# Optimization experiments

Measured on AMD Instinct MI355X. Metric: run time of the kernel, lower is better.

## Reference

```python
import jax, jax.numpy as jnp
import numpy as np
from jax import lax

B, S, I = 128, 256, 128          # batch, seq_len, input_size
CTX, OUT = 256, 128              # context_input_size, output_size
CPM, NM = 1024, 4                # center_size_per_module, num_modules
CENTER = NM * CPM
IN_SIZES = [I + CTX, CTX, CTX, CTX]          # only module 0 sees the input
HID = [CPM, CPM, CPM, CPM + OUT]             # last module also emits output


def setup_inputs() -> dict:
    key = jax.random.key(0)
    ks = jax.random.split(key, 4 + 5 * NM)
    d = {
        "inputs": jax.random.normal(ks[0], (B, 1, S, I), jnp.float32),
        "center_init": jax.random.normal(ks[1], (NM, B, CPM), jnp.float32),
        "mod_init": jax.random.normal(ks[2], (NM - 1, B, CPM), jnp.float32),
        "mod_init_last": jax.random.normal(ks[3], (B, CPM + OUT), jnp.float32),
    }
    for i in range(NM):
        k = ks[4 + 5 * i: 4 + 5 * (i + 1)]
        d[f"pm{i}"] = jax.random.normal(k[0], (CENTER, CTX), jnp.float32) * 0.02
        d[f"wih{i}"] = jax.random.normal(k[1], (3 * HID[i], IN_SIZES[i]), jnp.float32) * 0.05
        d[f"whh{i}"] = jax.random.normal(k[2], (3 * HID[i], HID[i]), jnp.float32) * 0.05
        d[f"bih{i}"] = jnp.zeros((3 * HID[i],), jnp.float32)
        d[f"bhh{i}"] = jnp.zeros((3 * HID[i],), jnp.float32)
    return d


def _gru(x, h, wih, whh, bih, bhh):
    # PyTorch GRUCell semantics
    gi = x @ wih.T + bih
    gh = h @ whh.T + bhh
    ir, iz, inn = jnp.split(gi, 3, axis=1)
    hr, hz, hn = jnp.split(gh, 3, axis=1)
    r = jax.nn.sigmoid(ir + hr)
    z = jax.nn.sigmoid(iz + hz)
    n = jnp.tanh(inn + r * hn)
    return (1.0 - z) * n + z * h


def _forward(inputs, center_init, mod_init, mod_init_last, pms, wihs, whhs, bihs, bhhs):
    xs = jnp.swapaxes(inputs[:, 0], 0, 1)  # [S, B, I]

    def step(carry, x_t):
        centers, mods, mod_last = carry  # [NM,B,CPM], [NM-1,B,CPM], [B,CPM+OUT]
        # torch.cat(prev_center_states, dim=1): module-major concat -> [B, NM*CPM]
        center_state = jnp.reshape(jnp.swapaxes(centers, 0, 1), (centers.shape[1], -1))
        new_centers, new_mods = [], []
        out = new_mod_last = None
        for i in range(NM):
            ctx = center_state @ pms[i]                       # [B, CTX]
            xin = jnp.concatenate([x_t, ctx], axis=1) if i == 0 else ctx
            h_prev = mod_last if i == NM - 1 else mods[i]
            h = _gru(xin, h_prev, wihs[i], whhs[i], bihs[i], bhhs[i])
            if i == NM - 1:
                out = h[:, :OUT]                              # split([output, center_feat])
                new_centers.append(h[:, OUT:])
                new_mod_last = h
            else:
                new_centers.append(h)
                new_mods.append(h)
        return (jnp.stack(new_centers), jnp.stack(new_mods), new_mod_last), out

    _, ys = lax.scan(step, (center_init, mod_init, mod_init_last), xs)
    return jnp.swapaxes(ys, 0, 1)  # [B, S, OUT]


def reference(inputs, center_init, mod_init, mod_init_last,
              pm0, pm1, pm2, pm3,
              wih0, wih1, wih2, wih3,
              whh0, whh1, whh2, whh3,
              bih0, bih1, bih2, bih3,
              bhh0, bhh1, bhh2, bhh3):
    return _forward(inputs, center_init, mod_init, mod_init_last,
                    (pm0, pm1, pm2, pm3),
                    (wih0, wih1, wih2, wih3),
                    (whh0, whh1, whh2, whh3),
                    (bih0, bih1, bih2, bih3),
                    (bhh0, bhh1, bhh2, bhh3))
```

## Files before the change

### kernel.cpp

```cpp
#include <hip/hip_runtime.h>
#include <hip/hip_bf16.h>

typedef _Float16 f16;
typedef f16  f16x8 __attribute__((ext_vector_type(8)));
typedef float f32x4 __attribute__((ext_vector_type(4)));

__device__ __forceinline__ f16x8 ld8h(const f16* p){ return *reinterpret_cast<const f16x8*>(p); }
__device__ __forceinline__ void fsplit(float x, f16* hi, f16* lo){
    f16 h=(f16)x; *hi=h; *lo=(f16)((x-(float)h)*4096.0f);
}
__device__ __forceinline__ size_t fragoff(int n, int k, int Kc){
    return ((size_t)(n>>4)*Kc + (k>>5))*512 + (size_t)((((k&31)>>3)*16 + (n&15))*8 + (k&7));
}

constexpr size_t NXE   = 128ull*256*128;
constexpr size_t NPM   = 1024ull*4096;
constexpr size_t NWIH0 = 3072ull*384;
constexpr size_t NWIH12= 3072ull*256;
constexpr size_t NWIH3 = 3456ull*256;
constexpr size_t NWHH  = 3072ull*1024;
constexpr size_t NWHH3 = 3456ull*1152;
constexpr size_t NCEN  = 128ull*4096;
constexpr size_t NCTX  = 128ull*1024;
constexpr size_t NHMX  = 128ull*1152;

constexpr size_t OFF_XH    = 0;
constexpr size_t OFF_XL    = OFF_XH + NXE*2;
constexpr size_t OFF_PMH   = OFF_XL + NXE*2;
constexpr size_t OFF_PML   = OFF_PMH + NPM*2;
constexpr size_t OFF_WIHH0 = OFF_PML + NPM*2;
constexpr size_t OFF_WIHH1 = OFF_WIHH0 + NWIH0*2;
constexpr size_t OFF_WIHH2 = OFF_WIHH1 + NWIH12*2;
constexpr size_t OFF_WIHH3 = OFF_WIHH2 + NWIH12*2;
constexpr size_t OFF_WIHL0 = OFF_WIHH3 + NWIH3*2;
constexpr size_t OFF_WIHL1 = OFF_WIHL0 + NWIH0*2;
constexpr size_t OFF_WIHL2 = OFF_WIHL1 + NWIH12*2;
constexpr size_t OFF_WIHL3 = OFF_WIHL2 + NWIH12*2;
constexpr size_t OFF_WHHH0 = OFF_WIHL3 + NWIH3*2;
constexpr size_t OFF_WHHH1 = OFF_WHHH0 + NWHH*2;
constexpr size_t OFF_WHHH2 = OFF_WHHH1 + NWHH*2;
constexpr size_t OFF_WHHH3 = OFF_WHHH2 + NWHH*2;
constexpr size_t OFF_WHHL0 = OFF_WHHH3 + NWHH3*2;
constexpr size_t OFF_WHHL1 = OFF_WHHL0 + NWHH*2;
constexpr size_t OFF_WHHL2 = OFF_WHHL1 + NWHH*2;
constexpr size_t OFF_WHHL3 = OFF_WHHL2 + NWHH*2;
constexpr size_t OFF_CENH  = OFF_WHHL3 + NWHH3*2;
constexpr size_t OFF_CENL  = OFF_CENH + 2*NCEN*2;
constexpr size_t OFF_CTXH  = OFF_CENL + 2*NCEN*2;
constexpr size_t OFF_CTXL  = OFF_CTXH + NCTX*2;
constexpr size_t OFF_HH    = OFF_CTXL + NCTX*2;
constexpr size_t OFF_HL    = OFF_HH + 8*NHMX*2;
constexpr size_t OFF_HF    = OFF_HL + 8*NHMX*2;
constexpr size_t WS_NEED   = OFF_HF + 8*NHMX*4;

__device__ __forceinline__ f16* hh_ptr(char* ws,int p,int i){ return (f16*)(ws+OFF_HH+((size_t)(p*4+i))*NHMX*2); }
__device__ __forceinline__ f16* hl_ptr(char* ws,int p,int i){ return (f16*)(ws+OFF_HL+((size_t)(p*4+i))*NHMX*2); }
__device__ __forceinline__ float* hf_ptr(char* ws,int p,int i){ return (float*)(ws+OFF_HF+((size_t)(p*4+i))*NHMX*4); }

__global__ void k_repack_w(const float* __restrict__ src, f16* __restrict__ hi,
                           f16* __restrict__ lo, int K){
    int n = blockIdx.x;
    const float* row = src + (size_t)n*K;
    int Kc = K >> 5;
    for (int k8 = threadIdx.x*8; k8 < K; k8 += 2048) {
        f16x8 hv, lv;
        #pragma unroll
        for (int e = 0; e < 8; ++e) { f16 a,b; fsplit(row[k8+e], &a, &b); hv[e]=a; lv[e]=b; }
        size_t d = fragoff(n, k8, Kc);
        *reinterpret_cast<f16x8*>(hi + d) = hv;
        *reinterpret_cast<f16x8*>(lo + d) = lv;
    }
}

__global__ void k_repack_pm(const float* __restrict__ p0, const float* __restrict__ p1,
                            const float* __restrict__ p2, const float* __restrict__ p3,
                            f16* __restrict__ hi, f16* __restrict__ lo){
    int k0 = blockIdx.x * 8;
    for (int c = threadIdx.x; c < 1024; c += 256) {
        int i = c >> 8, nl = c & 255;
        const float* p = (i==0?p0 : i==1?p1 : i==2?p2 : p3);
        f16x8 hv, lv;
        #pragma unroll
        for (int e = 0; e < 8; ++e) { f16 a,b; fsplit(p[(size_t)(k0+e)*256 + nl], &a, &b); hv[e]=a; lv[e]=b; }
        #pragma unroll
        for (int e = 0; e < 8; ++e) { size_t d = fragoff(c, k0+e, 128); hi[d]=hv[e]; lo[d]=lv[e]; }
    }
}

__global__ void k_repack_x(const float* __restrict__ src, f16* __restrict__ hi, f16* __restrict__ lo){
    size_t g = ((size_t)blockIdx.x*256 + threadIdx.x) * 8;
    if (g >= NXE) return;
    int m = (int)(g >> 15), t = (int)((g >> 7) & 255), d0 = (int)(g & 127);
    f16x8 hv, lv;
    #pragma unroll
    for (int e = 0; e < 8; ++e) { f16 a,b; fsplit(src[g+e], &a, &b); hv[e]=a; lv[e]=b; }
    size_t d = (size_t)t*16384 + fragoff(m, d0, 4);
    *reinterpret_cast<f16x8*>(hi + d) = hv;
    *reinterpret_cast<f16x8*>(lo + d) = lv;
}

__global__ void k_init_cen(const float* __restrict__ ci, char* ws){
    size_t g = ((size_t)blockIdx.x*256 + threadIdx.x) * 8;
    if (g >= 4ull*128*1024) return;
    int i = (int)(g >> 17), b = (int)((g >> 10) & 127), c = (int)(g & 1023);
    f16* hi = (f16*)(ws + OFF_CENH);
    f16* lo = (f16*)(ws + OFF_CENL);
    f16x8 hv, lv;
    #pragma unroll
    for (int e = 0; e < 8; ++e) { f16 a,bb; fsplit(ci[g+e], &a, &bb); hv[e]=a; lv[e]=bb; }
    size_t d = fragoff(b, i*1024 + c, 128);
    *reinterpret_cast<f16x8*>(hi + d) = hv;
    *reinterpret_cast<f16x8*>(lo + d) = lv;
}

__global__ void k_init_mod(const float* __restrict__ mi, char* ws){
    size_t g = ((size_t)blockIdx.x*256 + threadIdx.x) * 8;
    if (g >= 3ull*128*1024) return;
    int i = (int)(g >> 17), b = (int)((g >> 10) & 127), j = (int)(g & 1023);
    float* hf = hf_ptr(ws, 0, i);
    f16 *hh = hh_ptr(ws, 0, i), *hl = hl_ptr(ws, 0, i);
    f16x8 hv, lv;
    #pragma unroll
    for (int e = 0; e < 8; ++e) {
        float v = mi[g+e]; hf[(size_t)b*1024 + j + e] = v;
        f16 a,bb; fsplit(v, &a, &bb); hv[e]=a; lv[e]=bb;
    }
    size_t d = fragoff(b, j, 32);
    *reinterpret_cast<f16x8*>(hh + d) = hv;
    *reinterpret_cast<f16x8*>(hl + d) = lv;
}

__global__ void k_init_last(const float* __restrict__ ml, char* ws){
    int b = blockIdx.x;
    float* hf = hf_ptr(ws, 0, 3);
    f16 *hh = hh_ptr(ws, 0, 3), *hl = hl_ptr(ws, 0, 3);
    for (int j = threadIdx.x*8; j < 1152; j += 2048) {
        f16x8 hv, lv;
        #pragma unroll
        for (int e = 0; e < 8; ++e) {
            float v = ml[(size_t)b*1152 + j + e]; hf[(size_t)b*1152 + j + e] = v;
            f16 a,bb; fsplit(v, &a, &bb); hv[e]=a; lv[e]=bb;
        }
        size_t d = fragoff(b, j, 36);
        *reinterpret_cast<f16x8*>(hh + d) = hv;
        *reinterpret_cast<f16x8*>(hl + d) = lv;
    }
}

__global__ __launch_bounds__(512) void k_ctx(char* ws, int par){
    __shared__ float red[8][32][17];
    const f16* cenh = (const f16*)(ws + OFF_CENH) + (size_t)par*NCEN;
    const f16* cenl = (const f16*)(ws + OFF_CENL) + (size_t)par*NCEN;
    const f16* pmh  = (const f16*)(ws + OFF_PMH);
    const f16* pml  = (const f16*)(ws + OFF_PML);
    int tid = threadIdx.x, lane = tid & 63, wv = tid >> 6;
    int bm = blockIdx.x >> 6, bn = blockIdx.x & 63;
    size_t lb = (size_t)lane*8;
    size_t a0 = ((size_t)(bm*2)*128 + wv*16)*512 + lb;
    size_t a1 = a0 + 128*512;
    size_t bb = ((size_t)bn*128 + wv*16)*512 + lb;
    f32x4 h0={},h1={},c0={},c1={};
    #pragma unroll 4
    for (int kc = 0; kc < 16; ++kc) {
        f16x8 bh = ld8h(pmh + bb + kc*512), bl = ld8h(pml + bb + kc*512);
        f16x8 ah0 = ld8h(cenh + a0 + kc*512), al0 = ld8h(cenl + a0 + kc*512);
        f16x8 ah1 = ld8h(cenh + a1 + kc*512), al1 = ld8h(cenl + a1 + kc*512);
        h0 = __builtin_amdgcn_mfma_f32_16x16x32_f16(ah0, bh, h0, 0,0,0);
        c0 = __builtin_amdgcn_mfma_f32_16x16x32_f16(al0, bh, c0, 0,0,0);
        c0 = __builtin_amdgcn_mfma_f32_16x16x32_f16(ah0, bl, c0, 0,0,0);
        h1 = __builtin_amdgcn_mfma_f32_16x16x32_f16(ah1, bh, h1, 0,0,0);
        c1 = __builtin_amdgcn_mfma_f32_16x16x32_f16(al1, bh, c1, 0,0,0);
        c1 = __builtin_amdgcn_mfma_f32_16x16x32_f16(ah1, bl, c1, 0,0,0);
    }
    int rg = lane >> 4, fr = lane & 15;
    const float inv = 1.0f/4096.0f;
    #pragma unroll
    for (int rr = 0; rr < 4; ++rr) {
        red[wv][rg*4+rr][fr]      = h0[rr] + c0[rr]*inv;
        red[wv][16+rg*4+rr][fr]   = h1[rr] + c1[rr]*inv;
    }
    __syncthreads();
    int r = tid >> 4, c = tid & 15;
    float s = red[0][r][c]+red[1][r][c]+red[2][r][c]+red[3][r][c]
            + red[4][r][c]+red[5][r][c]+red[6][r][c]+red[7][r][c];
    int m = bm*32 + r, n = bn*16 + c;
    size_t d = fragoff(m, n, 32);
    f16* ctxh = (f16*)(ws + OFF_CTXH);
    f16* ctxl = (f16*)(ws + OFF_CTXL);
    fsplit(s, &ctxh[d], &ctxl[d]);
}

__global__ __launch_bounds__(256) void k_fused(char* ws,
    const float* __restrict__ bih0, const float* __restrict__ bih1,
    const float* __restrict__ bih2, const float* __restrict__ bih3,
    const float* __restrict__ bhh0, const float* __restrict__ bhh1,
    const float* __restrict__ bhh2, const float* __restrict__ bhh3,
    float* __restrict__ out, int t, int par)
{
    int tid = threadIdx.x, lane = tid & 63, wv = tid >> 6;
    int fr = lane & 15, rg = lane >> 4;
    int tile = blockIdx.x;
    int i, jt;
    if (tile < 64)       { i = 0; jt = tile; }
    else if (tile < 128) { i = 1; jt = tile - 64; }
    else if (tile < 192) { i = 2; jt = tile - 128; }
    else                 { i = 3; jt = tile - 192; }
    const int H  = (i == 3) ? 1152 : 1024;
    const int K1 = (i == 0) ? 384 : 256;
    const int Kc1 = K1 >> 5, KcH = H >> 5, Ht = H >> 4;

    const f16* WihH = (const f16*)(ws + (i==0?OFF_WIHH0 : i==1?OFF_WIHH1 : i==2?OFF_WIHH2 : OFF_WIHH3));
    const f16* WihL = (const f16*)(ws + (i==0?OFF_WIHL0 : i==1?OFF_WIHL1 : i==2?OFF_WIHL2 : OFF_WIHL3));
    const f16* WhhH = (const f16*)(ws + (i==0?OFF_WHHH0 : i==1?OFF_WHHH1 : i==2?OFF_WHHH2 : OFF_WHHH3));
    const f16* WhhL = (const f16*)(ws + (i==0?OFF_WHHL0 : i==1?OFF_WHHL1 : i==2?OFF_WHHL2 : OFF_WHHL3));

    size_t lb = (size_t)lane*8;
    size_t b1[3], b2[3];
    #pragma unroll
    for (int s = 0; s < 3; ++s) {
        b1[s] = ((size_t)(s*Ht + jt)*Kc1)*512 + lb;
        b2[s] = ((size_t)(s*Ht + jt)*KcH)*512 + lb;
    }
    int mt0 = wv*2;
    f32x4 aRh[2]={{},{}}, aRc[2]={{},{}}, aZh[2]={{},{}}, aZc[2]={{},{}};
    f32x4 aIh[2]={{},{}}, aIc[2]={{},{}}, aNh[2]={{},{}}, aNc[2]={{},{}};

    {
        const f16* XH_ = (const f16*)(ws + OFF_XH);
        const f16* XL_ = (const f16*)(ws + OFF_XL);
        const f16* CH_ = (const f16*)(ws + OFF_CTXH);
        const f16* CL_ = (const f16*)(ws + OFF_CTXL);
        size_t xb0 = ((size_t)(t*8 + mt0)*4)*512 + lb, xb1 = xb0 + 4*512;
        size_t cb0 = ((size_t)mt0*32)*512 + lb,        cb1 = cb0 + 32*512;
        #pragma unroll 2
        for (int kc = 0; kc < Kc1; ++kc) {
            f16x8 ah0, al0, ah1, al1;
            if (i == 0 && kc < 4) {
                ah0 = ld8h(XH_ + xb0 + kc*512); al0 = ld8h(XL_ + xb0 + kc*512);
                ah1 = ld8h(XH_ + xb1 + kc*512); al1 = ld8h(XL_ + xb1 + kc*512);
            } else {
                int ck = (i == 0) ? kc - 4 : i*8 + kc;
                ah0 = ld8h(CH_ + cb0 + ck*512); al0 = ld8h(CL_ + cb0 + ck*512);
                ah1 = ld8h(CH_ + cb1 + ck*512); al1 = ld8h(CL_ + cb1 + ck*512);
            }
            f16x8 bh, bl;
            bh = ld8h(WihH + b1[0] + kc*512); bl = ld8h(WihL + b1[0] + kc*512);
            aRh[0] = __builtin_amdgcn_mfma_f32_16x16x32_f16(ah0, bh, aRh[0],0,0,0);
            aRc[0] = __builtin_amdgcn_mfma_f32_16x16x32_f16(al0, bh, aRc[0],0,0,0);
            aRc[0] = __builtin_amdgcn_mfma_f32_16x16x32_f16(ah0, bl, aRc[0],0,0,0);
            aRh[1] = __builtin_amdgcn_mfma_f32_16x16x32_f16(ah1, bh, aRh[1],0,0,0);
            aRc[1] = __builtin_amdgcn_mfma_f32_16x16x32_f16(al1, bh, aRc[1],0,0,0);
            aRc[1] = __builtin_amdgcn_mfma_f32_16x16x32_f16(ah1, bl, aRc[1],0,0,0);
            bh = ld8h(WihH + b1[1] + kc*512); bl = ld8h(WihL + b1[1] + kc*512);
            aZh[0] = __builtin_amdgcn_mfma_f32_16x16x32_f16(ah0, bh, aZh[0],0,0,0);
            aZc[0] = __builtin_amdgcn_mfma_f32_16x16x32_f16(al0, bh, aZc[0],0,0,0);
            aZc[0] = __builtin_amdgcn_mfma_f32_16x16x32_f16(ah0, bl, aZc[0],0,0,0);
            aZh[1] = __builtin_amdgcn_mfma_f32_16x16x32_f16(ah1, bh, aZh[1],0,0,0);
            aZc[1] = __builtin_amdgcn_mfma_f32_16x16x32_f16(al1, bh, aZc[1],0,0,0);
            aZc[1] = __builtin_amdgcn_mfma_f32_16x16x32_f16(ah1, bl, aZc[1],0,0,0);
            bh = ld8h(WihH + b1[2] + kc*512); bl = ld8h(WihL + b1[2] + kc*512);
            aIh[0] = __builtin_amdgcn_mfma_f32_16x16x32_f16(ah0, bh, aIh[0],0,0,0);
            aIc[0] = __builtin_amdgcn_mfma_f32_16x16x32_f16(al0, bh, aIc[0],0,0,0);
            aIc[0] = __builtin_amdgcn_mfma_f32_16x16x32_f16(ah0, bl, aIc[0],0,0,0);
            aIh[1] = __builtin_amdgcn_mfma_f32_16x16x32_f16(ah1, bh, aIh[1],0,0,0);
            aIc[1] = __builtin_amdgcn_mfma_f32_16x16x32_f16(al1, bh, aIc[1],0,0,0);
            aIc[1] = __builtin_amdgcn_mfma_f32_16x16x32_f16(ah1, bl, aIc[1],0,0,0);
        }
    }
    {
        const f16* HHp = hh_ptr(ws, par, i);
        const f16* HLp = hl_ptr(ws, par, i);
        size_t hb0 = ((size_t)mt0*KcH)*512 + lb, hb1 = hb0 + (size_t)KcH*512;
        #pragma unroll 2
        for (int kc = 0; kc < KcH; ++kc) {
            f16x8 ah0 = ld8h(HHp + hb0 + kc*512), al0 = ld8h(HLp + hb0 + kc*512);
            f16x8 ah1 = ld8h(HHp + hb1 + kc*512), al1 = ld8h(HLp + hb1 + kc*512);
            f16x8 bh, bl;
            bh = ld8h(WhhH + b2[0] + kc*512); bl = ld8h(WhhL + b2[0] + kc*512);
            aRh[0] = __builtin_amdgcn_mfma_f32_16x16x32_f16(ah0, bh, aRh[0],0,0,0);
            aRc[0] = __builtin_amdgcn_mfma_f32_16x16x32_f16(al0, bh, aRc[0],0,0,0);
            aRc[0] = __builtin_amdgcn_mfma_f32_16x16x32_f16(ah0, bl, aRc[0],0,0,0);
            aRh[1] = __builtin_amdgcn_mfma_f32_16x16x32_f16(ah1, bh, aRh[1],0,0,0);
            aRc[1] = __builtin_amdgcn_mfma_f32_16x16x32_f16(al1, bh, aRc[1],0,0,0);
            aRc[1] = __builtin_amdgcn_mfma_f32_16x16x32_f16(ah1, bl, aRc[1],0,0,0);
            bh = ld8h(WhhH + b2[1] + kc*512); bl = ld8h(WhhL + b2[1] + kc*512);
            aZh[0] = __builtin_amdgcn_mfma_f32_16x16x32_f16(ah0, bh, aZh[0],0,0,0);
            aZc[0] = __builtin_amdgcn_mfma_f32_16x16x32_f16(al0, bh, aZc[0],0,0,0);
            aZc[0] = __builtin_amdgcn_mfma_f32_16x16x32_f16(ah0, bl, aZc[0],0,0,0);
            aZh[1] = __builtin_amdgcn_mfma_f32_16x16x32_f16(ah1, bh, aZh[1],0,0,0);
            aZc[1] = __builtin_amdgcn_mfma_f32_16x16x32_f16(al1, bh, aZc[1],0,0,0);
            aZc[1] = __builtin_amdgcn_mfma_f32_16x16x32_f16(ah1, bl, aZc[1],0,0,0);
            bh = ld8h(WhhH + b2[2] + kc*512); bl = ld8h(WhhL + b2[2] + kc*512);
            aNh[0] = __builtin_amdgcn_mfma_f32_16x16x32_f16(ah0, bh, aNh[0],0,0,0);
            aNc[0] = __builtin_amdgcn_mfma_f32_16x16x32_f16(al0, bh, aNc[0],0,0,0);
            aNc[0] = __builtin_amdgcn_mfma_f32_16x16x32_f16(ah0, bl, aNc[0],0,0,0);
            aNh[1] = __builtin_amdgcn_mfma_f32_16x16x32_f16(ah1, bh, aNh[1],0,0,0);
            aNc[1] = __builtin_amdgcn_mfma_f32_16x16x32_f16(al1, bh, aNc[1],0,0,0);
            aNc[1] = __builtin_amdgcn_mfma_f32_16x16x32_f16(ah1, bl, aNc[1],0,0,0);
        }
    }

    const float* bihp = (i==0?bih0 : i==1?bih1 : i==2?bih2 : bih3);
    const float* bhhp = (i==0?bhh0 : i==1?bhh1 : i==2?bhh2 : bhh3);
    int j = jt*16 + fr;
    float bir = bihp[j], biz = bihp[H+j], bin = bihp[2*H+j];
    float bhr = bhhp[j], bhz = bhhp[H+j], bhn = bhhp[2*H+j];
    const float* hfP = hf_ptr(ws, par, i);
    float* hfN = hf_ptr(ws, par^1, i);
    f16 *hhN = hh_ptr(ws, par^1, i), *hlN = hl_ptr(ws, par^1, i);
    f16* cenhN = (f16*)(ws + OFF_CENH) + (size_t)(par^1)*NCEN;
    f16* cenlN = (f16*)(ws + OFF_CENL) + (size_t)(par^1)*NCEN;
    const float inv = 1.0f/4096.0f;
    #pragma unroll
    for (int mf = 0; mf < 2; ++mf) {
        #pragma unroll
        for (int rr = 0; rr < 4; ++rr) {
            float r_ = aRh[mf][rr] + aRc[mf][rr]*inv + bir + bhr;
            float z_ = aZh[mf][rr] + aZc[mf][rr]*inv + biz + bhz;
            float in_ = aIh[mf][rr] + aIc[mf][rr]*inv + bin;
            float hn_ = aNh[mf][rr] + aNc[mf][rr]*inv + bhn;
            float rgt = 1.f/(1.f + expf(-r_));
            float zgt = 1.f/(1.f + expf(-z_));
            float ngt = tanhf(in_ + rgt*hn_);
            int m = wv*32 + mf*16 + rg*4 + rr;
            float hp = hfP[(size_t)m*H + j];
            float hnew = (1.f - zgt)*ngt + zgt*hp;
            hfN[(size_t)m*H + j] = hnew;
            size_t hd = fragoff(m, j, KcH);
            fsplit(hnew, &hhN[hd], &hlN[hd]);
            if (i < 3) {
                size_t cd = fragoff(m, i*1024 + j, 128);
                fsplit(hnew, &cenhN[cd], &cenlN[cd]);
            } else if (j >= 128) {
                size_t cd = fragoff(m, 3072 + j - 128, 128);
                fsplit(hnew, &cenhN[cd], &cenlN[cd]);
            } else {
                out[((size_t)m*256 + t)*128 + j] = hnew;
            }
        }
    }
}

extern "C" void kernel_launch(void* const* d_in, const int* in_sizes, int n_in,
                              void* d_out, int out_size, void* d_ws, size_t ws_size,
                              hipStream_t stream)
{
    char* ws = (char*)d_ws;
    const float* inp   = (const float*)d_in[0];
    const float* cini  = (const float*)d_in[1];
    const float* mini  = (const float*)d_in[2];
    const float* mlast = (const float*)d_in[3];
    const float *pm[4], *wih[4], *whh[4], *bih[4], *bhh[4];
    for (int i = 0; i < 4; ++i) {
        pm[i]  = (const float*)d_in[4 + 5*i];
        wih[i] = (const float*)d_in[5 + 5*i];
        whh[i] = (const float*)d_in[6 + 5*i];
        bih[i] = (const float*)d_in[7 + 5*i];
        bhh[i] = (const float*)d_in[8 + 5*i];
    }
    float* out = (float*)d_out;

    k_repack_x<<<2048, 256, 0, stream>>>(inp, (f16*)(ws+OFF_XH), (f16*)(ws+OFF_XL));
    k_repack_pm<<<512, 256, 0, stream>>>(pm[0], pm[1], pm[2], pm[3],
                                         (f16*)(ws+OFF_PMH), (f16*)(ws+OFF_PML));
    k_repack_w<<<3072, 256, 0, stream>>>(wih[0], (f16*)(ws+OFF_WIHH0), (f16*)(ws+OFF_WIHL0), 384);
    k_repack_w<<<3072, 256, 0, stream>>>(wih[1], (f16*)(ws+OFF_WIHH1), (f16*)(ws+OFF_WIHL1), 256);
    k_repack_w<<<3072, 256, 0, stream>>>(wih[2], (f16*)(ws+OFF_WIHH2), (f16*)(ws+OFF_WIHL2), 256);
    k_repack_w<<<3456, 256, 0, stream>>>(wih[3], (f16*)(ws+OFF_WIHH3), (f16*)(ws+OFF_WIHL3), 256);
    k_repack_w<<<3072, 256, 0, stream>>>(whh[0], (f16*)(ws+OFF_WHHH0), (f16*)(ws+OFF_WHHL0), 1024);
    k_repack_w<<<3072, 256, 0, stream>>>(whh[1], (f16*)(ws+OFF_WHHH1), (f16*)(ws+OFF_WHHL1), 1024);
    k_repack_w<<<3072, 256, 0, stream>>>(whh[2], (f16*)(ws+OFF_WHHH2), (f16*)(ws+OFF_WHHL2), 1024);
    k_repack_w<<<3456, 256, 0, stream>>>(whh[3], (f16*)(ws+OFF_WHHH3), (f16*)(ws+OFF_WHHL3), 1152);
    k_init_cen<<<256, 256, 0, stream>>>(cini, ws);
    k_init_mod<<<192, 256, 0, stream>>>(mini, ws);
    k_init_last<<<128, 256, 0, stream>>>(mlast, ws);

    for (int t = 0; t < 256; ++t) {
        int par = t & 1;
        k_ctx<<<256, 512, 0, stream>>>(ws, par);
        k_fused<<<264, 256, 0, stream>>>(ws,
            bih[0], bih[1], bih[2], bih[3],
            bhh[0], bhh[1], bhh[2], bhh[3],
            out, t, par);
    }
    (void)in_sizes; (void)n_in; (void)out_size; (void)ws_size; (void)WS_NEED;
}
```

Baseline: 14.59 ms.

## Replace per-timestep kernel launches with persistent cooperative kernel using grid syncs

Replaces the 512 per-step kernel launches (context matmul plus fused GRU gates) with one cooperative persistent kernel of 512 blocks that loops over all timesteps, separating the phases with grid-wide syncs. Work is re-split so each block computes one 16x16 context tile and half of a gate tile (one 16-row fragment per wave); 16 blocks take an extra gate unit. This is meant to remove launch overhead and the inter-kernel gaps on the serial recurrence. In exchange it adds two grid syncs per step, halves the M-reuse of each loaded weight fragment in the gate phase, and leaves the extra gate units on a few blocks as a tail.

```diff
diff --git a/kernel.cpp b/kernel.cpp
--- a/kernel.cpp
+++ b/kernel.cpp
@@ -1,5 +1,8 @@
 #include <hip/hip_runtime.h>
 #include <hip/hip_bf16.h>
+#include <hip/hip_cooperative_groups.h>
+
+namespace cg = cooperative_groups;
 
 typedef _Float16 f16;
 typedef f16  f16x8 __attribute__((ext_vector_type(8)));
@@ -9,6 +12,7 @@
 __device__ __forceinline__ void fsplit(float x, f16* hi, f16* lo){
     f16 h=(f16)x; *hi=h; *lo=(f16)((x-(float)h)*4096.0f);
 }
+#define MFMA16(a,b,c) __builtin_amdgcn_mfma_f32_16x16x32_f16((a),(b),(c),0,0,0)
 __device__ __forceinline__ size_t fragoff(int n, int k, int Kc){
     return ((size_t)(n>>4)*Kc + (k>>5))*512 + (size_t)((((k&31)>>3)*16 + (n&15))*8 + (k&7));
 }
@@ -79,11 +83,11 @@
     for (int c = threadIdx.x; c < 1024; c += 256) {
         int i = c >> 8, nl = c & 255;
         const float* p = (i==0?p0 : i==1?p1 : i==2?p2 : p3);
-        f16x8 hv, lv;
         #pragma unroll
-        for (int e = 0; e < 8; ++e) { f16 a,b; fsplit(p[(size_t)(k0+e)*256 + nl], &a, &b); hv[e]=a; lv[e]=b; }
-        #pragma unroll
-        for (int e = 0; e < 8; ++e) { size_t d = fragoff(c, k0+e, 128); hi[d]=hv[e]; lo[d]=lv[e]; }
+        for (int e = 0; e < 8; ++e) {
+            f16 a,b; fsplit(p[(size_t)(k0+e)*256 + nl], &a, &b);
+            size_t d = fragoff(c, k0+e, 128); hi[d]=a; lo[d]=b;
+        }
     }
 }
 
@@ -147,59 +151,13 @@
     }
 }
 
-__global__ __launch_bounds__(512) void k_ctx(char* ws, int par){
-    __shared__ float red[8][32][17];
-    const f16* cenh = (const f16*)(ws + OFF_CENH) + (size_t)par*NCEN;
-    const f16* cenl = (const f16*)(ws + OFF_CENL) + (size_t)par*NCEN;
-    const f16* pmh  = (const f16*)(ws + OFF_PMH);
-    const f16* pml  = (const f16*)(ws + OFF_PML);
-    int tid = threadIdx.x, lane = tid & 63, wv = tid >> 6;
-    int bm = blockIdx.x >> 6, bn = blockIdx.x & 63;
-    size_t lb = (size_t)lane*8;
-    size_t a0 = ((size_t)(bm*2)*128 + wv*16)*512 + lb;
-    size_t a1 = a0 + 128*512;
-    size_t bb = ((size_t)bn*128 + wv*16)*512 + lb;
-    f32x4 h0={},h1={},c0={},c1={};
-    #pragma unroll 4
-    for (int kc = 0; kc < 16; ++kc) {
-        f16x8 bh = ld8h(pmh + bb + kc*512), bl = ld8h(pml + bb + kc*512);
-        f16x8 ah0 = ld8h(cenh + a0 + kc*512), al0 = ld8h(cenl + a0 + kc*512);
-        f16x8 ah1 = ld8h(cenh + a1 + kc*512), al1 = ld8h(cenl + a1 + kc*512);
-        h0 = __builtin_amdgcn_mfma_f32_16x16x32_f16(ah0, bh, h0, 0,0,0);
-        c0 = __builtin_amdgcn_mfma_f32_16x16x32_f16(al0, bh, c0, 0,0,0);
-        c0 = __builtin_amdgcn_mfma_f32_16x16x32_f16(ah0, bl, c0, 0,0,0);
-        h1 = __builtin_amdgcn_mfma_f32_16x16x32_f16(ah1, bh, h1, 0,0,0);
-        c1 = __builtin_amdgcn_mfma_f32_16x16x32_f16(al1, bh, c1, 0,0,0);
-        c1 = __builtin_amdgcn_mfma_f32_16x16x32_f16(ah1, bl, c1, 0,0,0);
-    }
-    int rg = lane >> 4, fr = lane & 15;
-    const float inv = 1.0f/4096.0f;
-    #pragma unroll
-    for (int rr = 0; rr < 4; ++rr) {
-        red[wv][rg*4+rr][fr]      = h0[rr] + c0[rr]*inv;
-        red[wv][16+rg*4+rr][fr]   = h1[rr] + c1[rr]*inv;
-    }
-    __syncthreads();
-    int r = tid >> 4, c = tid & 15;
-    float s = red[0][r][c]+red[1][r][c]+red[2][r][c]+red[3][r][c]
-            + red[4][r][c]+red[5][r][c]+red[6][r][c]+red[7][r][c];
-    int m = bm*32 + r, n = bn*16 + c;
-    size_t d = fragoff(m, n, 32);
-    f16* ctxh = (f16*)(ws + OFF_CTXH);
-    f16* ctxl = (f16*)(ws + OFF_CTXL);
-    fsplit(s, &ctxh[d], &ctxl[d]);
-}
-
-__global__ __launch_bounds__(256) void k_fused(char* ws,
-    const float* __restrict__ bih0, const float* __restrict__ bih1,
-    const float* __restrict__ bih2, const float* __restrict__ bih3,
-    const float* __restrict__ bhh0, const float* __restrict__ bhh1,
-    const float* __restrict__ bhh2, const float* __restrict__ bhh3,
-    float* __restrict__ out, int t, int par)
+__device__ __forceinline__ void gates_unit(char* ws,
+    const float* bih0, const float* bih1, const float* bih2, const float* bih3,
+    const float* bhh0, const float* bhh1, const float* bhh2, const float* bhh3,
+    float* out, int t, int par, int u, int lane, int wv)
 {
-    int tid = threadIdx.x, lane = tid & 63, wv = tid >> 6;
-    int fr = lane & 15, rg = lane >> 4;
-    int tile = blockIdx.x;
+    int tile = (u < 512) ? (u >> 1) : (256 + ((u - 512) >> 1));
+    int half = u & 1;
     int i, jt;
     if (tile < 64)       { i = 0; jt = tile; }
     else if (tile < 128) { i = 1; jt = tile - 64; }
@@ -221,85 +179,49 @@
         b1[s] = ((size_t)(s*Ht + jt)*Kc1)*512 + lb;
         b2[s] = ((size_t)(s*Ht + jt)*KcH)*512 + lb;
     }
-    int mt0 = wv*2;
-    f32x4 aRh[2]={{},{}}, aRc[2]={{},{}}, aZh[2]={{},{}}, aZc[2]={{},{}};
-    f32x4 aIh[2]={{},{}}, aIc[2]={{},{}}, aNh[2]={{},{}}, aNc[2]={{},{}};
+    int mf = half*4 + wv;
+
+    f32x4 rh={},rc={},zh={},zc={},inh={},inc={},nhh={},nhc={};
 
     {
         const f16* XH_ = (const f16*)(ws + OFF_XH);
         const f16* XL_ = (const f16*)(ws + OFF_XL);
         const f16* CH_ = (const f16*)(ws + OFF_CTXH);
         const f16* CL_ = (const f16*)(ws + OFF_CTXL);
-        size_t xb0 = ((size_t)(t*8 + mt0)*4)*512 + lb, xb1 = xb0 + 4*512;
-        size_t cb0 = ((size_t)mt0*32)*512 + lb,        cb1 = cb0 + 32*512;
+        size_t xb = ((size_t)(t*8 + mf)*4)*512 + lb;
+        size_t cb = ((size_t)mf*32)*512 + lb;
         #pragma unroll 2
         for (int kc = 0; kc < Kc1; ++kc) {
-            f16x8 ah0, al0, ah1, al1;
-            if (i == 0 && kc < 4) {
-                ah0 = ld8h(XH_ + xb0 + kc*512); al0 = ld8h(XL_ + xb0 + kc*512);
-                ah1 = ld8h(XH_ + xb1 + kc*512); al1 = ld8h(XL_ + xb1 + kc*512);
-            } else {
-                int ck = (i == 0) ? kc - 4 : i*8 + kc;
-                ah0 = ld8h(CH_ + cb0 + ck*512); al0 = ld8h(CL_ + cb0 + ck*512);
-                ah1 = ld8h(CH_ + cb1 + ck*512); al1 = ld8h(CL_ + cb1 + ck*512);
-            }
+            f16x8 ah, al;
+            if (i == 0 && kc < 4) { ah = ld8h(XH_ + xb + kc*512); al = ld8h(XL_ + xb + kc*512); }
+            else { int ck = (i == 0) ? kc - 4 : i*8 + kc;
+                   ah = ld8h(CH_ + cb + ck*512); al = ld8h(CL_ + cb + ck*512); }
             f16x8 bh, bl;
             bh = ld8h(WihH + b1[0] + kc*512); bl = ld8h(WihL + b1[0] + kc*512);
-            aRh[0] = __builtin_amdgcn_mfma_f32_16x16x32_f16(ah0, bh, aRh[0],0,0,0);
-            aRc[0] = __builtin_amdgcn_mfma_f32_16x16x32_f16(al0, bh, aRc[0],0,0,0);
-            aRc[0] = __builtin_amdgcn_mfma_f32_16x16x32_f16(ah0, bl, aRc[0],0,0,0);
-            aRh[1] = __builtin_amdgcn_mfma_f32_16x16x32_f16(ah1, bh, aRh[1],0,0,0);
-            aRc[1] = __builtin_amdgcn_mfma_f32_16x16x32_f16(al1, bh, aRc[1],0,0,0);
-            aRc[1] = __builtin_amdgcn_mfma_f32_16x16x32_f16(ah1, bl, aRc[1],0,0,0);
+            rh = MFMA16(ah,bh,rh); rc = MFMA16(al,bh,rc); rc = MFMA16(ah,bl,rc);
             bh = ld8h(WihH + b1[1] + kc*512); bl = ld8h(WihL + b1[1] + kc*512);
-            aZh[0] = __builtin_amdgcn_mfma_f32_16x16x32_f16(ah0, bh, aZh[0],0,0,0);
-            aZc[0] = __builtin_amdgcn_mfma_f32_16x16x32_f16(al0, bh, aZc[0],0,0,0);
-            aZc[0] = __builtin_amdgcn_mfma_f32_16x16x32_f16(ah0, bl, aZc[0],0,0,0);
-            aZh[1] = __builtin_amdgcn_mfma_f32_16x16x32_f16(ah1, bh, aZh[1],0,0,0);
-            aZc[1] = __builtin_amdgcn_mfma_f32_16x16x32_f16(al1, bh, aZc[1],0,0,0);
-            aZc[1] = __builtin_amdgcn_mfma_f32_16x16x32_f16(ah1, bl, aZc[1],0,0,0);
+            zh = MFMA16(ah,bh,zh); zc = MFMA16(al,bh,zc); zc = MFMA16(ah,bl,zc);
             bh = ld8h(WihH + b1[2] + kc*512); bl = ld8h(WihL + b1[2] + kc*512);
-            aIh[0] = __builtin_amdgcn_mfma_f32_16x16x32_f16(ah0, bh, aIh[0],0,0,0);
-            aIc[0] = __builtin_amdgcn_mfma_f32_16x16x32_f16(al0, bh, aIc[0],0,0,0);
-            aIc[0] = __builtin_amdgcn_mfma_f32_16x16x32_f16(ah0, bl, aIc[0],0,0,0);
-            aIh[1] = __builtin_amdgcn_mfma_f32_16x16x32_f16(ah1, bh, aIh[1],0,0,0);
-            aIc[1] = __builtin_amdgcn_mfma_f32_16x16x32_f16(al1, bh, aIc[1],0,0,0);
-            aIc[1] = __builtin_amdgcn_mfma_f32_16x16x32_f16(ah1, bl, aIc[1],0,0,0);
+            inh = MFMA16(ah,bh,inh); inc = MFMA16(al,bh,inc); inc = MFMA16(ah,bl,inc);
         }
     }
     {
         const f16* HHp = hh_ptr(ws, par, i);
         const f16* HLp = hl_ptr(ws, par, i);
-        size_t hb0 = ((size_t)mt0*KcH)*512 + lb, hb1 = hb0 + (size_t)KcH*512;
+        size_t hb = ((size_t)mf*KcH)*512 + lb;
         #pragma unroll 2
         for (int kc = 0; kc < KcH; ++kc) {
-            f16x8 ah0 = ld8h(HHp + hb0 + kc*512), al0 = ld8h(HLp + hb0 + kc*512);
-            f16x8 ah1 = ld8h(HHp + hb1 + kc*512), al1 = ld8h(HLp + hb1 + kc*512);
+            f16x8 ah = ld8h(HHp + hb + kc*512), al = ld8h(HLp + hb + kc*512);
             f16x8 bh, bl;
             bh = ld8h(WhhH + b2[0] + kc*512); bl = ld8h(WhhL + b2[0] + kc*512);
-            aRh[0] = __builtin_amdgcn_mfma_f32_16x16x32_f16(ah0, bh, aRh[0],0,0,0);
-            aRc[0] = __builtin_amdgcn_mfma_f32_16x16x32_f16(al0, bh, aRc[0],0,0,0);
-            aRc[0] = __builtin_amdgcn_mfma_f32_16x16x32_f16(ah0, bl, aRc[0],0,0,0);
-            aRh[1] = __builtin_amdgcn_mfma_f32_16x16x32_f16(ah1, bh, aRh[1],0,0,0);
-            aRc[1] = __builtin_amdgcn_mfma_f32_16x16x32_f16(al1, bh, aRc[1],0,0,0);
-            aRc[1] = __builtin_amdgcn_mfma_f32_16x16x32_f16(ah1, bl, aRc[1],0,0,0);
+            rh = MFMA16(ah,bh,rh); rc = MFMA16(al,bh,rc); rc = MFMA16(ah,bl,rc);
             bh = ld8h(WhhH + b2[1] + kc*512); bl = ld8h(WhhL + b2[1] + kc*512);
-            aZh[0] = __builtin_amdgcn_mfma_f32_16x16x32_f16(ah0, bh, aZh[0],0,0,0);
-            aZc[0] = __builtin_amdgcn_mfma_f32_16x16x32_f16(al0, bh, aZc[0],0,0,0);
-            aZc[0] = __builtin_amdgcn_mfma_f32_16x16x32_f16(ah0, bl, aZc[0],0,0,0);
-            aZh[1] = __builtin_amdgcn_mfma_f32_16x16x32_f16(ah1, bh, aZh[1],0,0,0);
-            aZc[1] = __builtin_amdgcn_mfma_f32_16x16x32_f16(al1, bh, aZc[1],0,0,0);
-            aZc[1] = __builtin_amdgcn_mfma_f32_16x16x32_f16(ah1, bl, aZc[1],0,0,0);
+            zh = MFMA16(ah,bh,zh); zc = MFMA16(al,bh,zc); zc = MFMA16(ah,bl,zc);
             bh = ld8h(WhhH + b2[2] + kc*512); bl = ld8h(WhhL + b2[2] + kc*512);
-            aNh[0] = __builtin_amdgcn_mfma_f32_16x16x32_f16(ah0, bh, aNh[0],0,0,0);
-            aNc[0] = __builtin_amdgcn_mfma_f32_16x16x32_f16(al0, bh, aNc[0],0,0,0);
-            aNc[0] = __builtin_amdgcn_mfma_f32_16x16x32_f16(ah0, bl, aNc[0],0,0,0);
-            aNh[1] = __builtin_amdgcn_mfma_f32_16x16x32_f16(ah1, bh, aNh[1],0,0,0);
-            aNc[1] = __builtin_amdgcn_mfma_f32_16x16x32_f16(al1, bh, aNc[1],0,0,0);
-            aNc[1] = __builtin_amdgcn_mfma_f32_16x16x32_f16(ah1, bl, aNc[1],0,0,0);
-        }
-    }
-
+            nhh = MFMA16(ah,bh,nhh); nhc = MFMA16(al,bh,nhc); nhc = MFMA16(ah,bl,nhc);
+        }
+    }
+    int rg = lane >> 4, fr = lane & 15;
     const float* bihp = (i==0?bih0 : i==1?bih1 : i==2?bih2 : bih3);
     const float* bhhp = (i==0?bhh0 : i==1?bhh1 : i==2?bhh2 : bhh3);
     int j = jt*16 + fr;
@@ -312,32 +234,80 @@
     f16* cenlN = (f16*)(ws + OFF_CENL) + (size_t)(par^1)*NCEN;
     const float inv = 1.0f/4096.0f;
     #pragma unroll
-    for (int mf = 0; mf < 2; ++mf) {
-        #pragma unroll
-        for (int rr = 0; rr < 4; ++rr) {
-            float r_ = aRh[mf][rr] + aRc[mf][rr]*inv + bir + bhr;
-            float z_ = aZh[mf][rr] + aZc[mf][rr]*inv + biz + bhz;
-            float in_ = aIh[mf][rr] + aIc[mf][rr]*inv + bin;
-            float hn_ = aNh[mf][rr] + aNc[mf][rr]*inv + bhn;
-            float rgt = 1.f/(1.f + expf(-r_));
-            float zgt = 1.f/(1.f + expf(-z_));
-            float ngt = tanhf(in_ + rgt*hn_);
-            int m = wv*32 + mf*16 + rg*4 + rr;
-            float hp = hfP[(size_t)m*H + j];
-            float hnew = (1.f - zgt)*ngt + zgt*hp;
-            hfN[(size_t)m*H + j] = hnew;
-            size_t hd = fragoff(m, j, KcH);
-            fsplit(hnew, &hhN[hd], &hlN[hd]);
-            if (i < 3) {
-                size_t cd = fragoff(m, i*1024 + j, 128);
-                fsplit(hnew, &cenhN[cd], &cenlN[cd]);
-            } else if (j >= 128) {
-                size_t cd = fragoff(m, 3072 + j - 128, 128);
-                fsplit(hnew, &cenhN[cd], &cenlN[cd]);
-            } else {
-                out[((size_t)m*256 + t)*128 + j] = hnew;
+    for (int rr = 0; rr < 4; ++rr) {
+        float r_  = rh[rr]  + rc[rr]*inv  + bir + bhr;
+        float z_  = zh[rr]  + zc[rr]*inv  + biz + bhz;
+        float in_ = inh[rr] + inc[rr]*inv + bin;
+        float hn_ = nhh[rr] + nhc[rr]*inv + bhn;
+        float rgt = 1.f/(1.f + expf(-r_));
+        float zgt = 1.f/(1.f + expf(-z_));
+        float ngt = tanhf(in_ + rgt*hn_);
+        int m = half*64 + wv*16 + rg*4 + rr;
+        float hp = hfP[(size_t)m*H + j];
+        float hnew = (1.f - zgt)*ngt + zgt*hp;
+        hfN[(size_t)m*H + j] = hnew;
+        size_t hd = fragoff(m, j, KcH);
+        fsplit(hnew, &hhN[hd], &hlN[hd]);
+        if (i < 3) {
+            size_t cd = fragoff(m, i*1024 + j, 128);
+            fsplit(hnew, &cenhN[cd], &cenlN[cd]);
+        } else if (j >= 128) {
+            size_t cd = fragoff(m, 3072 + j - 128, 128);
+            fsplit(hnew, &cenhN[cd], &cenlN[cd]);
+        } else {
+            out[((size_t)m*256 + t)*128 + j] = hnew;
+        }
+    }
+}
+
+__global__ __launch_bounds__(256, 2) void k_persist(char* ws,
+    const float* __restrict__ bih0, const float* __restrict__ bih1,
+    const float* __restrict__ bih2, const float* __restrict__ bih3,
+    const float* __restrict__ bhh0, const float* __restrict__ bhh1,
+    const float* __restrict__ bhh2, const float* __restrict__ bhh3,
+    float* __restrict__ out)
+{
+    cg::grid_group grid = cg::this_grid();
+    __shared__ float red[4][16][17];
+    const int tid = threadIdx.x, lane = tid & 63, wv = tid >> 6;
+    const int bid = blockIdx.x;
+    const size_t lb = (size_t)lane*8;
+    const f16* pmh = (const f16*)(ws + OFF_PMH);
+    const f16* pml = (const f16*)(ws + OFF_PML);
+    f16* ctxh = (f16*)(ws + OFF_CTXH);
+    f16* ctxl = (f16*)(ws + OFF_CTXL);
+    const int bm = bid >> 6, bn = bid & 63;
+
+    for (int t = 0; t < 256; ++t) {
+        const int par = t & 1;
+        {
+            const f16* cenh = (const f16*)(ws + OFF_CENH) + (size_t)par*NCEN;
+            const f16* cenl = (const f16*)(ws + OFF_CENL) + (size_t)par*NCEN;
+            size_t ab = ((size_t)bm*128 + wv*32)*512 + lb;
+            size_t bb = ((size_t)bn*128 + wv*32)*512 + lb;
+            f32x4 h = {}, c = {};
+            #pragma unroll 4
+            for (int kc = 0; kc < 32; ++kc) {
+                f16x8 ah = ld8h(cenh + ab + kc*512), al = ld8h(cenl + ab + kc*512);
+                f16x8 bh = ld8h(pmh + bb + kc*512),  bl = ld8h(pml + bb + kc*512);
+                h = MFMA16(ah,bh,h); c = MFMA16(al,bh,c); c = MFMA16(ah,bl,c);
             }
-        }
+            int rg = lane >> 4, fr = lane & 15;
+            const float inv = 1.0f/4096.0f;
+            #pragma unroll
+            for (int rr = 0; rr < 4; ++rr)
+                red[wv][rg*4+rr][fr] = h[rr] + c[rr]*inv;
+            __syncthreads();
+            int r = tid >> 4, cc = tid & 15;
+            float s = red[0][r][cc] + red[1][r][cc] + red[2][r][cc] + red[3][r][cc];
+            size_t d = fragoff(bm*16 + r, bn*16 + cc, 32);
+            fsplit(s, &ctxh[d], &ctxl[d]);
+        }
+        grid.sync();
+        gates_unit(ws, bih0,bih1,bih2,bih3, bhh0,bhh1,bhh2,bhh3, out, t, par, bid, lane, wv);
+        if (bid < 16)
+            gates_unit(ws, bih0,bih1,bih2,bih3, bhh0,bhh1,bhh2,bhh3, out, t, par, 512 + bid, lane, wv);
+        grid.sync();
     }
 }
 
@@ -375,13 +345,12 @@
     k_init_mod<<<192, 256, 0, stream>>>(mini, ws);
     k_init_last<<<128, 256, 0, stream>>>(mlast, ws);
 
-    for (int t = 0; t < 256; ++t) {
-        int par = t & 1;
-        k_ctx<<<256, 512, 0, stream>>>(ws, par);
-        k_fused<<<264, 256, 0, stream>>>(ws,
-            bih[0], bih[1], bih[2], bih[3],
-            bhh[0], bhh[1], bhh[2], bhh[3],
-            out, t, par);
-    }
+    char* wsp = ws;
+    const float *b0 = bih[0], *b1 = bih[1], *b2 = bih[2], *b3 = bih[3];
+    const float *h0 = bhh[0], *h1 = bhh[1], *h2 = bhh[2], *h3 = bhh[3];
+    float* outp = out;
+    void* args[] = { &wsp, &b0, &b1, &b2, &b3, &h0, &h1, &h2, &h3, &outp };
+    hipLaunchCooperativeKernel(reinterpret_cast<void*>(k_persist),
+                               dim3(512), dim3(256), args, 0, stream);
     (void)in_sizes; (void)n_in; (void)out_size; (void)ws_size; (void)WS_NEED;
 }
```

New measurement: 48.18 ms. 3.3x slower.
